# Kernel tuning notes

Hardware: AMD Instinct MI355X
Metric: run time of the kernel (lower is better)

The kernel has to match this reference:

```python
import jax, jax.numpy as jnp
import numpy as np

N_HEADS = 16
HEAD_SIZE = 64
SEQ_LEN = 2048
EMBED = 1024
BATCH = 2


def setup_inputs() -> dict:
    key = jax.random.key(0)
    ks = jax.random.split(key, 9)
    d_inner = N_HEADS * HEAD_SIZE
    s = 1.0 / np.sqrt(EMBED)
    inp = {
        "inputs": jax.random.normal(ks[0], (BATCH, SEQ_LEN, EMBED), jnp.float32),
        "Wq": jax.random.uniform(ks[1], (EMBED, d_inner), jnp.float32, -s, s),
        "bq": jax.random.uniform(ks[2], (d_inner,), jnp.float32, -s, s),
        "Wk": jax.random.uniform(ks[3], (EMBED, d_inner), jnp.float32, -s, s),
        "bk": jax.random.uniform(ks[4], (d_inner,), jnp.float32, -s, s),
        "Wv": jax.random.uniform(ks[5], (EMBED, d_inner), jnp.float32, -s, s),
        "bv": jax.random.uniform(ks[6], (d_inner,), jnp.float32, -s, s),
        "Wo": jax.random.uniform(ks[7], (d_inner, EMBED), jnp.float32, -s, s),
        "bo": jax.random.uniform(ks[8], (EMBED,), jnp.float32, -s, s),
    }
    return inp


def reference(inputs, Wq, bq, Wk, bk, Wv, bv, Wo, bo):
    B, S, _ = inputs.shape
    # QKV projections -> [B, H, S, Dh]
    def proj(W, b):
        return (inputs @ W + b).reshape(B, S, N_HEADS, HEAD_SIZE).transpose(0, 2, 1, 3)
    q, k, v = proj(Wq, bq), proj(Wk, bk), proj(Wv, bv)
    scores = jnp.einsum("bhqd,bhkd->bhqk", q, k) / jnp.sqrt(jnp.float32(HEAD_SIZE))
    causal = jnp.tril(jnp.ones((S, S), dtype=bool))  # [S, S]
    scores = jnp.where(causal[None, None], scores, -jnp.inf)
    attn = jax.nn.softmax(scores, axis=-1)  # dropout is identity in eval
    out = jnp.einsum("bhqk,bhkd->bhqd", attn, v)
    out = out.transpose(0, 2, 1, 3).reshape(B, S, N_HEADS * HEAD_SIZE)
    return out @ Wo + bo
```

## Files before the change

### kernel.cpp

```cpp
#include <hip/hip_runtime.h>
#include <hip/hip_bf16.h>
#include <math.h>

#define NH 16
#define DH 64
#define SEQ 2048
#define EMBED 1024
#define DINNER 1024
#define BATCH 2
#define MTOK 4096

typedef __bf16 bf16x8 __attribute__((ext_vector_type(8)));
typedef float  f32x4  __attribute__((ext_vector_type(4)));
typedef float  f32x16 __attribute__((ext_vector_type(16)));
typedef unsigned int u32;

__device__ __forceinline__ void gload16(const void* g, void* l) {
    __builtin_amdgcn_global_load_lds((const __attribute__((address_space(1))) void*)g,
                                     (__attribute__((address_space(3))) void*)l, 16, 0, 0);
}

__global__ __launch_bounds__(256) void cvt_bf16(
    const float* __restrict__ src, __bf16* __restrict__ dst, int n)
{
    int i = (blockIdx.x * 256 + threadIdx.x) * 4;
    if (i + 3 < n) {
        float4 v = *(const float4*)&src[i];
        dst[i + 0] = (__bf16)v.x;
        dst[i + 1] = (__bf16)v.y;
        dst[i + 2] = (__bf16)v.z;
        dst[i + 3] = (__bf16)v.w;
    }
}

__global__ __launch_bounds__(256) void tconv4(
    const float* __restrict__ W0, const float* __restrict__ W1,
    const float* __restrict__ W2, const float* __restrict__ W3,
    __bf16* __restrict__ D0, __bf16* __restrict__ D1,
    __bf16* __restrict__ D2, __bf16* __restrict__ D3)
{
    const int z = blockIdx.z;
    const float* __restrict__ src = (z == 0) ? W0 : (z == 1) ? W1 : (z == 2) ? W2 : W3;
    __bf16* __restrict__ dst      = (z == 0) ? D0 : (z == 1) ? D1 : (z == 2) ? D2 : D3;
    const int R = 1024, C = 1024;

    __shared__ float t[32][33];
    const int c0 = blockIdx.x * 32, r0 = blockIdx.y * 32;
    const int x = threadIdx.x & 31, y = threadIdx.x >> 5;
#pragma unroll
    for (int i = 0; i < 4; ++i)
        t[y + 8 * i][x] = src[(size_t)(r0 + y + 8 * i) * C + c0 + x];
    __syncthreads();
#pragma unroll
    for (int i = 0; i < 4; ++i)
        dst[(size_t)(c0 + y + 8 * i) * R + r0 + x] = (__bf16)t[x][y + 8 * i];
}

#define QSCALE 0.18033688f

__global__ __launch_bounds__(256) void gemm128(
    const __bf16* __restrict__ A,
    const __bf16* __restrict__ Bt0, const __bf16* __restrict__ Bt1, const __bf16* __restrict__ Bt2,
    const float* __restrict__ b0, const float* __restrict__ b1, const float* __restrict__ b2,
    void* __restrict__ o0, void* __restrict__ o1, void* __restrict__ o2,
    int Kdim, int mode3)
{
    const int z = blockIdx.z;
    const __bf16* __restrict__ Bt = (z == 0) ? Bt0 : (z == 1) ? Bt1 : Bt2;
    const float*  __restrict__ bias = (z == 0) ? b0 : (z == 1) ? b1 : b2;
    void* __restrict__ outp = (z == 0) ? o0 : (z == 1) ? o1 : o2;
    const int mode = mode3 ? 3 : z;

    __shared__ __bf16 As[128 * 32];
    __shared__ __bf16 Bs[128 * 32];

    const int tid  = threadIdx.x;
    const int lane = tid & 63;
    const int wid  = tid >> 6;
    const int wm = wid >> 1, wn = wid & 1;
    const int ls = lane & 15, lg = lane >> 4;
    const int m0 = blockIdx.y * 128, n0 = blockIdx.x * 128;

    const int sr = tid >> 2;
    const int sc = (tid & 3) * 8;

    f32x4 acc[4][4] = {};

    for (int k0 = 0; k0 < Kdim; k0 += 32) {
        gload16(&A [(size_t)(m0 + sr)      * Kdim + k0 + sc], &As[sr * 32 + sc]);
        gload16(&A [(size_t)(m0 + 64 + sr) * Kdim + k0 + sc], &As[(64 + sr) * 32 + sc]);
        gload16(&Bt[(size_t)(n0 + sr)      * Kdim + k0 + sc], &Bs[sr * 32 + sc]);
        gload16(&Bt[(size_t)(n0 + 64 + sr) * Kdim + k0 + sc], &Bs[(64 + sr) * 32 + sc]);
        __syncthreads();

        bf16x8 af[4], bfr[4];
#pragma unroll
        for (int i = 0; i < 4; ++i) {
            af[i]  = *(const bf16x8*)&As[(wm * 64 + i * 16 + ls) * 32 + lg * 8];
            bfr[i] = *(const bf16x8*)&Bs[(wn * 64 + i * 16 + ls) * 32 + lg * 8];
        }
#pragma unroll
        for (int i = 0; i < 4; ++i)
#pragma unroll
            for (int jx = 0; jx < 4; ++jx)
                acc[i][jx] = __builtin_amdgcn_mfma_f32_16x16x32_bf16(af[i], bfr[jx], acc[i][jx], 0, 0, 0);
        __syncthreads();
    }

#pragma unroll
    for (int i = 0; i < 4; ++i) {
#pragma unroll
        for (int jx = 0; jx < 4; ++jx) {
            const int mbase = m0 + wm * 64 + i * 16 + lg * 4;
            const int n = n0 + wn * 64 + jx * 16 + ls;
            if (mode == 3) {
#pragma unroll
                for (int j = 0; j < 4; ++j)
                    ((float*)outp)[(size_t)(mbase + j) * EMBED + n] = acc[i][jx][j] + bias[n];
            } else if (mode == 2) {
                const int b = mbase >> 11, s = mbase & 2047;
                const int h = n >> 6, d = n & 63;
                __bf16 t4[4];
#pragma unroll
                for (int j = 0; j < 4; ++j) t4[j] = (__bf16)(acc[i][jx][j] + bias[n]);
                *(uint2*)&((__bf16*)outp)[(((size_t)(b * NH + h) * DH + d) << 11) + s] = *(uint2*)t4;
            } else {
                const float sc2 = (mode == 0) ? QSCALE : 1.0f;
#pragma unroll
                for (int j = 0; j < 4; ++j) {
                    const int m = mbase + j;
                    const int b = m >> 11, s = m & 2047;
                    const int h = n >> 6, d = n & 63;
                    ((__bf16*)outp)[((((size_t)(b * NH + h) << 11) + s) * DH) + d] =
                        (__bf16)((acc[i][jx][j] + bias[n]) * sc2);
                }
            }
        }
    }
}

__global__ __launch_bounds__(64) void attn_mfma(
    const __bf16* __restrict__ Q, const __bf16* __restrict__ K,
    const __bf16* __restrict__ Vt, __bf16* __restrict__ ctx)
{
    __shared__ __bf16 lds[8192];

    const int lane = threadIdx.x & 63;
    const int col  = lane & 31;
    const int hi   = lane >> 5;
    const int bh   = blockIdx.x & 31;
    const int qt32 = 63 - (blockIdx.x >> 5);
    const int qlo  = qt32 * 32;
    const int b = bh >> 4, h = bh & 15;

    const __bf16* __restrict__ Qb = Q + ((size_t)bh << 11) * DH;
    const char* __restrict__ Kg = (const char*)(K  + ((size_t)bh << 11) * DH);
    const char* __restrict__ Vg = (const char*)(Vt + ((size_t)bh << 11) * DH);

    char* ldsK = (char*)&lds[0];
    char* ldsV = ldsK + 8192;

    const int srow = lane >> 3;
    const int sswz = ((lane & 7) * 16) ^ (srow << 4);
    const int swz  = (col & 7) << 4;

    bf16x8 qf[4];
#pragma unroll
    for (int c = 0; c < 4; ++c)
        qf[c] = *(const bf16x8*)&Qb[(size_t)(qlo + col) * DH + c * 16 + hi * 8];

    const int nt = (qt32 + 2) >> 1;

#pragma unroll
    for (int i = 0; i < 8; ++i)
        gload16(Kg + (size_t)(i * 8 + srow) * 128 + sswz, ldsK + i * 1024 + lane * 16);
#pragma unroll
    for (int i = 0; i < 8; ++i)
        gload16(Vg + (size_t)(i * 8 + srow) * 4096 + sswz, ldsV + i * 1024 + lane * 16);

    f32x16 oT0 = {}, oT1 = {};
    float mrun = 0.f, lrun = 0.f;

    for (int t = 0; t < nt; ++t) {
        const int k0 = t * 64;

        asm volatile("s_waitcnt vmcnt(8)" ::: "memory");

        bf16x8 kfa[4], kfb[4];
#pragma unroll
        for (int c = 0; c < 4; ++c) {
            kfa[c] = *(const bf16x8*)(ldsK + (     col) * 128 + ((c * 32 + hi * 16) ^ swz));
            kfb[c] = *(const bf16x8*)(ldsK + (32 + col) * 128 + ((c * 32 + hi * 16) ^ swz));
        }

        __builtin_amdgcn_s_setprio(1);
        f32x16 sta = {}, stb = {};
#pragma unroll
        for (int c = 0; c < 4; ++c) {
            sta = __builtin_amdgcn_mfma_f32_32x32x16_bf16(kfa[c], qf[c], sta, 0, 0, 0);
            stb = __builtin_amdgcn_mfma_f32_32x32x16_bf16(kfb[c], qf[c], stb, 0, 0, 0);
        }
        __builtin_amdgcn_s_setprio(0);

        asm volatile("s_waitcnt lgkmcnt(0)" ::: "memory");
        __builtin_amdgcn_sched_barrier(0);
        if (t + 1 < nt) {
            const int kbn = (t + 1) * 64;
#pragma unroll
            for (int i = 0; i < 8; ++i)
                gload16(Kg + (size_t)(kbn + i * 8 + srow) * 128 + sswz,
                        ldsK + i * 1024 + lane * 16);
        }

        if (k0 + 63 > qlo) {
#pragma unroll
            for (int r = 0; r < 16; ++r) {
                const int krel = (r & 3) + 8 * (r >> 2) + 4 * hi;
                if (k0 + krel > qlo + col)      sta[r] = -INFINITY;
                if (k0 + 32 + krel > qlo + col) stb[r] = -INFINITY;
            }
        }

        if (t == 0) {
            float ta = fmaxf(fmaxf(fmaxf(sta[0], sta[1]), fmaxf(sta[2], sta[3])),
                             fmaxf(fmaxf(sta[4], sta[5]), fmaxf(sta[6], sta[7])));
            float tb = fmaxf(fmaxf(fmaxf(sta[8], sta[9]),  fmaxf(sta[10], sta[11])),
                             fmaxf(fmaxf(sta[12], sta[13]), fmaxf(sta[14], sta[15])));
            float tc = fmaxf(fmaxf(fmaxf(stb[0], stb[1]), fmaxf(stb[2], stb[3])),
                             fmaxf(fmaxf(stb[4], stb[5]), fmaxf(stb[6], stb[7])));
            float td = fmaxf(fmaxf(fmaxf(stb[8], stb[9]),  fmaxf(stb[10], stb[11])),
                             fmaxf(fmaxf(stb[12], stb[13]), fmaxf(stb[14], stb[15])));
            float tmax = fmaxf(fmaxf(ta, tb), fmaxf(tc, td));
            tmax = fmaxf(tmax, __shfl_xor(tmax, 32));
            mrun = tmax;
        }

        float pa[16], pb[16];
#pragma unroll
        for (int r = 0; r < 16; ++r) { pa[r] = exp2f(sta[r] - mrun); pb[r] = exp2f(stb[r] - mrun); }
        float psa = (((pa[0] + pa[1]) + (pa[2] + pa[3])) + ((pa[4] + pa[5]) + (pa[6] + pa[7])))
                  + (((pa[8] + pa[9]) + (pa[10] + pa[11])) + ((pa[12] + pa[13]) + (pa[14] + pa[15])));
        float psb = (((pb[0] + pb[1]) + (pb[2] + pb[3])) + ((pb[4] + pb[5]) + (pb[6] + pb[7])))
                  + (((pb[8] + pb[9]) + (pb[10] + pb[11])) + ((pb[12] + pb[13]) + (pb[14] + pb[15])));
        float psum = psa + psb;
        psum += __shfl_xor(psum, 32);
        lrun += psum;

        u32 wa[8], wb[8];
#pragma unroll
        for (int i = 0; i < 8; ++i) {
            u32 r1, r2;
            asm("v_cvt_pk_bf16_f32 %0, %1, %2" : "=v"(r1) : "v"(pa[2 * i]), "v"(pa[2 * i + 1]));
            asm("v_cvt_pk_bf16_f32 %0, %1, %2" : "=v"(r2) : "v"(pb[2 * i]), "v"(pb[2 * i + 1]));
            wa[i] = r1; wb[i] = r2;
        }
        asm("v_permlane32_swap_b32 %0, %1" : "+v"(wa[0]), "+v"(wa[2]));
        asm("v_permlane32_swap_b32 %0, %1" : "+v"(wa[1]), "+v"(wa[3]));
        asm("v_permlane32_swap_b32 %0, %1" : "+v"(wa[4]), "+v"(wa[6]));
        asm("v_permlane32_swap_b32 %0, %1" : "+v"(wa[5]), "+v"(wa[7]));
        asm("v_permlane32_swap_b32 %0, %1" : "+v"(wb[0]), "+v"(wb[2]));
        asm("v_permlane32_swap_b32 %0, %1" : "+v"(wb[1]), "+v"(wb[3]));
        asm("v_permlane32_swap_b32 %0, %1" : "+v"(wb[4]), "+v"(wb[6]));
        asm("v_permlane32_swap_b32 %0, %1" : "+v"(wb[5]), "+v"(wb[7]));

        union { u32 u4[4]; bf16x8 v; } cA0, cA1, cB0, cB1;
        cA0.u4[0] = wa[0]; cA0.u4[1] = wa[1]; cA0.u4[2] = wa[2]; cA0.u4[3] = wa[3];
        cA1.u4[0] = wa[4]; cA1.u4[1] = wa[5]; cA1.u4[2] = wa[6]; cA1.u4[3] = wa[7];
        cB0.u4[0] = wb[0]; cB0.u4[1] = wb[1]; cB0.u4[2] = wb[2]; cB0.u4[3] = wb[3];
        cB1.u4[0] = wb[4]; cB1.u4[1] = wb[5]; cB1.u4[2] = wb[6]; cB1.u4[3] = wb[7];

        if (t + 1 < nt) { asm volatile("s_waitcnt vmcnt(8)" ::: "memory"); }
        else            { asm volatile("s_waitcnt vmcnt(0)" ::: "memory"); }

        __builtin_amdgcn_s_setprio(1);
#pragma unroll
        for (int dh = 0; dh < 2; ++dh) {
            bf16x8 v0 = *(const bf16x8*)(ldsV + (dh * 32 + col) * 128 + ((0  + hi * 16) ^ swz));
            bf16x8 v1 = *(const bf16x8*)(ldsV + (dh * 32 + col) * 128 + ((32 + hi * 16) ^ swz));
            bf16x8 v2 = *(const bf16x8*)(ldsV + (dh * 32 + col) * 128 + ((64 + hi * 16) ^ swz));
            bf16x8 v3 = *(const bf16x8*)(ldsV + (dh * 32 + col) * 128 + ((96 + hi * 16) ^ swz));
            f32x16& o = dh ? oT1 : oT0;
            o = __builtin_amdgcn_mfma_f32_32x32x16_bf16(v0, cA0.v, o, 0, 0, 0);
            o = __builtin_amdgcn_mfma_f32_32x32x16_bf16(v1, cA1.v, o, 0, 0, 0);
            o = __builtin_amdgcn_mfma_f32_32x32x16_bf16(v2, cB0.v, o, 0, 0, 0);
            o = __builtin_amdgcn_mfma_f32_32x32x16_bf16(v3, cB1.v, o, 0, 0, 0);
        }
        __builtin_amdgcn_s_setprio(0);

        asm volatile("s_waitcnt lgkmcnt(0)" ::: "memory");
        __builtin_amdgcn_sched_barrier(0);
        if (t + 1 < nt) {
            const int kbn = (t + 1) * 64;
#pragma unroll
            for (int i = 0; i < 8; ++i)
                gload16(Vg + (size_t)(i * 8 + srow) * 4096 + (size_t)kbn * 2 + sswz,
                        ldsV + i * 1024 + lane * 16);
        }
    }

    const float inv = 1.0f / lrun;
    const size_t base = ((size_t)(b * SEQ + qlo + col)) * DINNER + h * 64;
#pragma unroll
    for (int g = 0; g < 4; ++g) {
        __bf16 t4[4];
#pragma unroll
        for (int j = 0; j < 4; ++j) t4[j] = (__bf16)(oT0[4 * g + j] * inv);
        *(uint2*)&ctx[base + 8 * g + 4 * hi] = *(uint2*)t4;
#pragma unroll
        for (int j = 0; j < 4; ++j) t4[j] = (__bf16)(oT1[4 * g + j] * inv);
        *(uint2*)&ctx[base + 32 + 8 * g + 4 * hi] = *(uint2*)t4;
    }
}

extern "C" void kernel_launch(void* const* d_in, const int* in_sizes, int n_in,
                              void* d_out, int out_size, void* d_ws, size_t ws_size,
                              hipStream_t stream)
{
    const float* X  = (const float*)d_in[0];
    const float* Wq = (const float*)d_in[1];
    const float* bq = (const float*)d_in[2];
    const float* Wk = (const float*)d_in[3];
    const float* bk = (const float*)d_in[4];
    const float* Wv = (const float*)d_in[5];
    const float* bv = (const float*)d_in[6];
    const float* Wo = (const float*)d_in[7];
    const float* bo = (const float*)d_in[8];
    float* out = (float*)d_out;

    __bf16* ws  = (__bf16*)d_ws;
    const size_t MI = 1048576;
    __bf16* Xb   = ws;
    __bf16* Wtq  = ws + 4  * MI;
    __bf16* Wtk  = ws + 5  * MI;
    __bf16* Wtv  = ws + 6  * MI;
    __bf16* Wto  = ws + 7  * MI;
    __bf16* Qb   = ws + 8  * MI;
    __bf16* Kb   = ws + 12 * MI;
    __bf16* Vtb  = ws + 16 * MI;
    __bf16* ctxb = ws + 20 * MI;

    cvt_bf16<<<dim3(MTOK * EMBED / 1024), dim3(256), 0, stream>>>(X, Xb, MTOK * EMBED);
    tconv4<<<dim3(32, 32, 4), dim3(256), 0, stream>>>(Wq, Wk, Wv, Wo, Wtq, Wtk, Wtv, Wto);

    {
        dim3 grid(DINNER / 128, MTOK / 128, 3), blk(256);
        gemm128<<<grid, blk, 0, stream>>>(Xb, Wtq, Wtk, Wtv, bq, bk, bv,
                                          Qb, Kb, Vtb, EMBED, 0);
    }

    {
        dim3 grid(32 * (SEQ / 32)), blk(64);
        attn_mfma<<<grid, blk, 0, stream>>>(Qb, Kb, Vtb, ctxb);
    }

    {
        dim3 grid(EMBED / 128, MTOK / 128, 1), blk(256);
        gemm128<<<grid, blk, 0, stream>>>(ctxb, Wto, Wto, Wto, bo, bo, bo,
                                          out, out, out, DINNER, 1);
    }
}
```

Measured before the change: 140.3 us.

## Triple-buffer K/V tiles in LDS with two-tile prefetch in attention

The attention kernel moves from a single K/V LDS buffer to a three-slot ring buffer. It prefetches tiles two iterations ahead, using looser vmcnt waits and no lgkmcnt barrier before the async global-to-LDS loads. The goal is to hide more global-load latency behind the MFMA and softmax work. The cost is three times the LDS per single-wave block (48 KB), which sharply limits how many blocks fit on a CU. The prefetch condition also issues loads for one tile past the causal range on the last iterations, which may read beyond the head slice.

```diff
diff --git a/kernel.cpp b/kernel.cpp
--- a/kernel.cpp
+++ b/kernel.cpp
@@ -143,7 +143,7 @@
     const __bf16* __restrict__ Q, const __bf16* __restrict__ K,
     const __bf16* __restrict__ Vt, __bf16* __restrict__ ctx)
 {
-    __shared__ __bf16 lds[8192];
+    __shared__ __bf16 lds[3 * 8192];
 
     const int lane = threadIdx.x & 63;
     const int col  = lane & 31;
@@ -157,8 +157,7 @@
     const char* __restrict__ Kg = (const char*)(K  + ((size_t)bh << 11) * DH);
     const char* __restrict__ Vg = (const char*)(Vt + ((size_t)bh << 11) * DH);
 
-    char* ldsK = (char*)&lds[0];
-    char* ldsV = ldsK + 8192;
+    char* const base = (char*)&lds[0];
 
     const int srow = lane >> 3;
     const int sswz = ((lane & 7) * 16) ^ (srow << 4);
@@ -173,18 +172,29 @@
 
 #pragma unroll
     for (int i = 0; i < 8; ++i)
-        gload16(Kg + (size_t)(i * 8 + srow) * 128 + sswz, ldsK + i * 1024 + lane * 16);
+        gload16(Kg + (size_t)(i * 8 + srow) * 128 + sswz, base + i * 1024 + lane * 16);
 #pragma unroll
     for (int i = 0; i < 8; ++i)
-        gload16(Vg + (size_t)(i * 8 + srow) * 4096 + sswz, ldsV + i * 1024 + lane * 16);
+        gload16(Vg + (size_t)(i * 8 + srow) * 4096 + sswz, base + 8192 + i * 1024 + lane * 16);
+#pragma unroll
+    for (int i = 0; i < 8; ++i)
+        gload16(Kg + (size_t)(64 + i * 8 + srow) * 128 + sswz, base + 16384 + i * 1024 + lane * 16);
+#pragma unroll
+    for (int i = 0; i < 8; ++i)
+        gload16(Vg + (size_t)(i * 8 + srow) * 4096 + 128 + sswz, base + 16384 + 8192 + i * 1024 + lane * 16);
 
     f32x16 oT0 = {}, oT1 = {};
     float mrun = 0.f, lrun = 0.f;
 
+    int cur = 0;
     for (int t = 0; t < nt; ++t) {
         const int k0 = t * 64;
-
-        asm volatile("s_waitcnt vmcnt(8)" ::: "memory");
+        int nxt2 = cur + 2; if (nxt2 >= 3) nxt2 -= 3;
+        const bool more = (t + 2 <= nt);
+        char* ldsK = base + cur * 16384;
+        char* ldsV = ldsK + 8192;
+
+        asm volatile("s_waitcnt vmcnt(24)" ::: "memory");
 
         bf16x8 kfa[4], kfb[4];
 #pragma unroll
@@ -202,14 +212,12 @@
         }
         __builtin_amdgcn_s_setprio(0);
 
-        asm volatile("s_waitcnt lgkmcnt(0)" ::: "memory");
-        __builtin_amdgcn_sched_barrier(0);
-        if (t + 1 < nt) {
-            const int kbn = (t + 1) * 64;
+        if (more) {
+            const int kbn = (t + 2) * 64;
 #pragma unroll
             for (int i = 0; i < 8; ++i)
                 gload16(Kg + (size_t)(kbn + i * 8 + srow) * 128 + sswz,
-                        ldsK + i * 1024 + lane * 16);
+                        base + nxt2 * 16384 + i * 1024 + lane * 16);
         }
 
         if (k0 + 63 > qlo) {
@@ -269,8 +277,8 @@
         cB0.u4[0] = wb[0]; cB0.u4[1] = wb[1]; cB0.u4[2] = wb[2]; cB0.u4[3] = wb[3];
         cB1.u4[0] = wb[4]; cB1.u4[1] = wb[5]; cB1.u4[2] = wb[6]; cB1.u4[3] = wb[7];
 
-        if (t + 1 < nt) { asm volatile("s_waitcnt vmcnt(8)" ::: "memory"); }
-        else            { asm volatile("s_waitcnt vmcnt(0)" ::: "memory"); }
+        if (more) { asm volatile("s_waitcnt vmcnt(24)" ::: "memory"); }
+        else      { asm volatile("s_waitcnt vmcnt(16)" ::: "memory"); }
 
         __builtin_amdgcn_s_setprio(1);
 #pragma unroll
@@ -287,28 +295,30 @@
         }
         __builtin_amdgcn_s_setprio(0);
 
-        asm volatile("s_waitcnt lgkmcnt(0)" ::: "memory");
-        __builtin_amdgcn_sched_barrier(0);
-        if (t + 1 < nt) {
-            const int kbn = (t + 1) * 64;
+        if (more) {
+            const int kbn = (t + 2) * 64;
 #pragma unroll
             for (int i = 0; i < 8; ++i)
                 gload16(Vg + (size_t)(i * 8 + srow) * 4096 + (size_t)kbn * 2 + sswz,
-                        ldsV + i * 1024 + lane * 16);
-        }
-    }
+                        base + nxt2 * 16384 + 8192 + i * 1024 + lane * 16);
+        }
+
+        cur = (cur + 1 == 3) ? 0 : cur + 1;
+    }
+
+    asm volatile("s_waitcnt vmcnt(0)" ::: "memory");
 
     const float inv = 1.0f / lrun;
-    const size_t base = ((size_t)(b * SEQ + qlo + col)) * DINNER + h * 64;
+    const size_t obase = ((size_t)(b * SEQ + qlo + col)) * DINNER + h * 64;
 #pragma unroll
     for (int g = 0; g < 4; ++g) {
         __bf16 t4[4];
 #pragma unroll
         for (int j = 0; j < 4; ++j) t4[j] = (__bf16)(oT0[4 * g + j] * inv);
-        *(uint2*)&ctx[base + 8 * g + 4 * hi] = *(uint2*)t4;
+        *(uint2*)&ctx[obase + 8 * g + 4 * hi] = *(uint2*)t4;
 #pragma unroll
         for (int j = 0; j < 4; ++j) t4[j] = (__bf16)(oT1[4 * g + j] * inv);
-        *(uint2*)&ctx[base + 32 + 8 * g + 4 * hi] = *(uint2*)t4;
+        *(uint2*)&ctx[obase + 32 + 8 * g + 4 * hi] = *(uint2*)t4;
     }
 }
 
```

Result: slower. 166.2 us (+18.5%).
